# Kernel optimization log

Hardware: AMD Instinct MI355X
Metric: run time of the kernel (lower is better)

## Reference

```python
import jax, jax.numpy as jnp
import numpy as np

M, N, D, P = 16, 2048, 128, 8192
H = N // D  # 16
MAXLEN = 8448
EPS = 1e-5


def layernorm(x, g, b):
    mu = jnp.mean(x, axis=-1, keepdims=True)
    var = jnp.mean(jnp.square(x - mu), axis=-1, keepdims=True)
    return (x - mu) * jax.lax.rsqrt(var + EPS) * g + b


def setup_inputs() -> dict:
    key = jax.random.key(0)
    ks = jax.random.split(key, 10)
    s = 1.0 / np.sqrt(N)  # keep activations O(1) like trained weights
    return {
        "X": jax.random.normal(ks[0], (M, N), jnp.float32),
        "ln1_g": jnp.ones((N,), jnp.float32),
        "ln1_b": jnp.zeros((N,), jnp.float32),
        "Wq": jax.random.normal(ks[1], (N, N), jnp.float32) * s,
        "Wk": jax.random.normal(ks[2], (N, N), jnp.float32) * s,
        "Wv": jax.random.normal(ks[3], (N, N), jnp.float32) * s,
        "Wo": jax.random.normal(ks[4], (N, N), jnp.float32) * s,
        "ln2_g": jnp.ones((N,), jnp.float32),
        "ln2_b": jnp.zeros((N,), jnp.float32),
        "Wup": jax.random.normal(ks[5], (4 * N, N), jnp.float32) * s,
        "Wdown": jax.random.normal(ks[6], (N, 4 * N), jnp.float32) * (1.0 / np.sqrt(4 * N)),
        "cache_K": jax.random.normal(ks[7], (H, MAXLEN, D), jnp.float32),
        "cache_V": jax.random.normal(ks[8], (H, MAXLEN, D), jnp.float32),
    }


def reference(X, ln1_g, ln1_b, Wq, Wk, Wv, Wo, ln2_g, ln2_b, Wup, Wdown, cache_K, cache_V):
    residual = X
    Xn = layernorm(X, ln1_g, ln1_b)
    # torch Linear: y = x @ W.T
    q = (Xn @ Wq.T).reshape(M, H, D).transpose(1, 0, 2)  # (H,M,D)
    k = (Xn @ Wk.T).reshape(M, H, D).transpose(1, 0, 2)
    v = (Xn @ Wv.T).reshape(M, H, D).transpose(1, 0, 2)
    # KV-cache append
    cache_K = jax.lax.dynamic_update_slice(cache_K, k, (0, P, 0))
    cache_V = jax.lax.dynamic_update_slice(cache_V, v, (0, P, 0))
    Kc = cache_K[:, : P + M, :]  # (H,T,D), T = P+M
    Vc = cache_V[:, : P + M, :]
    scores = jnp.einsum("hmd,htd->hmt", q, Kc) / np.sqrt(D)
    weights = jax.nn.softmax(scores, axis=-1)
    attn = jnp.einsum("hmt,htd->hmd", weights, Vc)  # (H,M,D)
    attn = attn.transpose(1, 0, 2).reshape(M, N)
    X = residual + attn @ Wo.T
    residual = X
    Xn = layernorm(X, ln2_g, ln2_b)
    ffn = jax.nn.gelu(Xn @ Wup.T, approximate=False) @ Wdown.T
    return residual + ffn
```

## Files before the change

### kernel.cpp

```cpp
#include <hip/hip_runtime.h>
#include <hip/hip_bf16.h>
#include <math.h>

#define M_TOK 16
#define NDIM  2048
#define DHEAD 128
#define NHEAD 16
#define MAXLEN 8448
#define FFN   8192
#define TC    128
#define NCH   65
#define LN_EPS 1e-5f
#define RSQRT_D 0.08838834764831845f

template<int H>
__device__ __forceinline__ void fold_step(float* v, int lane, int o) {
    bool hi = (lane & o) != 0;
    #pragma unroll
    for (int i = 0; i < H; ++i) {
        float send = hi ? v[i] : v[i + H];
        float keep = hi ? v[i + H] : v[i];
        v[i] = keep + __shfl_xor(send, o);
    }
}

__device__ __forceinline__ void fold64(float* v, int lane) {
    fold_step<32>(v, lane, 32);
    fold_step<16>(v, lane, 16);
    fold_step<8>(v, lane, 8);
    fold_step<4>(v, lane, 4);
    fold_step<2>(v, lane, 2);
    fold_step<1>(v, lane, 1);
}

template<int KDIM>
__device__ __forceinline__ void gemv_splitk(const float* __restrict__ A,
                                            const float* __restrict__ W,
                                            int col0, int wid, int lane,
                                            float* v) {
    const int kbase = wid * (KDIM / 4);
    const float* wp = W + (size_t)col0 * KDIM + kbase + lane * 4;
    const float* ap = A + kbase + lane * 4;
    #pragma unroll 1
    for (int kc = 0; kc < KDIM / 4; kc += 256) {
        float4 w4[4];
        #pragma unroll
        for (int c = 0; c < 4; ++c)
            w4[c] = *(const float4*)(wp + (size_t)c * KDIM + kc);
        #pragma unroll
        for (int m = 0; m < 16; ++m) {
            float4 x4 = *(const float4*)(ap + (size_t)m * KDIM + kc);
            #pragma unroll
            for (int c = 0; c < 4; ++c) {
                v[m * 4 + c] = fmaf(w4[c].x, x4.x, v[m * 4 + c]);
                v[m * 4 + c] = fmaf(w4[c].y, x4.y, v[m * 4 + c]);
                v[m * 4 + c] = fmaf(w4[c].z, x4.z, v[m * 4 + c]);
                v[m * 4 + c] = fmaf(w4[c].w, x4.w, v[m * 4 + c]);
            }
        }
    }
}

__device__ __forceinline__ float crosswave_reduce(float val, int wid, int lane,
                                                  float (*s_red)[64]) {
    if (wid != 0) s_red[wid - 1][lane] = val;
    __syncthreads();
    return val + s_red[0][lane] + s_red[1][lane] + s_red[2][lane];
}

__global__ __launch_bounds__(256) void k_qkv(const float* __restrict__ Xn,
                                             const float* __restrict__ Wq,
                                             const float* __restrict__ Wk,
                                             const float* __restrict__ Wv,
                                             float* __restrict__ qws,
                                             float* __restrict__ kws,
                                             float* __restrict__ vws) {
    __shared__ float s_red[3][64];
    int tid = threadIdx.x, wid = tid >> 6, lane = tid & 63;
    int b = blockIdx.x;
    int sel = b >> 9;
    int cb = (b & 511) * 4;
    const float* W = (sel == 0) ? Wq : (sel == 1) ? Wk : Wv;
    float* dst = (sel == 0) ? qws : (sel == 1) ? kws : vws;
    float v[64];
    #pragma unroll
    for (int i = 0; i < 64; ++i) v[i] = 0.f;
    gemv_splitk<2048>(Xn, W, cb, wid, lane, v);
    fold64(v, lane);
    float r = crosswave_reduce(v[0], wid, lane, s_red);
    if (wid == 0) {
        int m = lane >> 2, c = lane & 3;
        int gcol = cb + c;
        int h = gcol >> 7, d = gcol & 127;
        dst[(((size_t)h * 16 + m) << 7) + d] = r;
    }
}

__device__ __forceinline__ float gelu_exact(float x) {
    return 0.5f * x * (1.0f + erff(x * 0.7071067811865475f));
}

__global__ __launch_bounds__(256) void k_up(const float* __restrict__ A,
                                            const float* __restrict__ W,
                                            float* __restrict__ out) {
    __shared__ float s_red[3][64];
    int tid = threadIdx.x, wid = tid >> 6, lane = tid & 63;
    int cb = blockIdx.x * 4;
    float v[64];
    #pragma unroll
    for (int i = 0; i < 64; ++i) v[i] = 0.f;
    gemv_splitk<2048>(A, W, cb, wid, lane, v);
    fold64(v, lane);
    float r = crosswave_reduce(v[0], wid, lane, s_red);
    if (wid == 0) {
        int m = lane >> 2, c = lane & 3;
        out[(size_t)m * FFN + cb + c] = gelu_exact(r);
    }
}

template<int KDIM>
__global__ __launch_bounds__(256) void k_resid(const float* __restrict__ A,
                                               const float* __restrict__ W,
                                               const float* __restrict__ R,
                                               float* __restrict__ out) {
    __shared__ float s_red[3][64];
    int tid = threadIdx.x, wid = tid >> 6, lane = tid & 63;
    int cb = blockIdx.x * 4;
    float v[64];
    #pragma unroll
    for (int i = 0; i < 64; ++i) v[i] = 0.f;
    gemv_splitk<KDIM>(A, W, cb, wid, lane, v);
    fold64(v, lane);
    float r = crosswave_reduce(v[0], wid, lane, s_red);
    if (wid == 0) {
        int m = lane >> 2, c = lane & 3;
        int col = cb + c;
        out[(size_t)m * NDIM + col] = R[(size_t)m * NDIM + col] + r;
    }
}

__global__ __launch_bounds__(256) void k_ln(const float* __restrict__ X,
                                            const float* __restrict__ g,
                                            const float* __restrict__ b,
                                            float* __restrict__ out) {
    int row = blockIdx.x, tid = threadIdx.x;
    const float4* xp = (const float4*)(X + (size_t)row * NDIM);
    float4 v0 = xp[tid], v1 = xp[tid + 256];
    float s = v0.x + v0.y + v0.z + v0.w + v1.x + v1.y + v1.z + v1.w;
    float q = v0.x*v0.x + v0.y*v0.y + v0.z*v0.z + v0.w*v0.w
            + v1.x*v1.x + v1.y*v1.y + v1.z*v1.z + v1.w*v1.w;
    #pragma unroll
    for (int o = 32; o; o >>= 1) { s += __shfl_xor(s, o); q += __shfl_xor(q, o); }
    __shared__ float ls[4], lq[4];
    int wid = tid >> 6, lane = tid & 63;
    if (lane == 0) { ls[wid] = s; lq[wid] = q; }
    __syncthreads();
    s = ls[0] + ls[1] + ls[2] + ls[3];
    q = lq[0] + lq[1] + lq[2] + lq[3];
    float mu  = s * (1.f / NDIM);
    float var = q * (1.f / NDIM) - mu * mu;
    float rs  = rsqrtf(var + LN_EPS);
    float4 g0 = ((const float4*)g)[tid], g1 = ((const float4*)g)[tid + 256];
    float4 b0 = ((const float4*)b)[tid], b1 = ((const float4*)b)[tid + 256];
    float4 o0, o1;
    o0.x = (v0.x - mu) * rs * g0.x + b0.x;  o0.y = (v0.y - mu) * rs * g0.y + b0.y;
    o0.z = (v0.z - mu) * rs * g0.z + b0.z;  o0.w = (v0.w - mu) * rs * g0.w + b0.w;
    o1.x = (v1.x - mu) * rs * g1.x + b1.x;  o1.y = (v1.y - mu) * rs * g1.y + b1.y;
    o1.z = (v1.z - mu) * rs * g1.z + b1.z;  o1.w = (v1.w - mu) * rs * g1.w + b1.w;
    float4* op = (float4*)(out + (size_t)row * NDIM);
    op[tid] = o0; op[tid + 256] = o1;
}

__global__ __launch_bounds__(256) void k_attn(const float* __restrict__ cacheK,
                                              const float* __restrict__ cacheV,
                                              const float* __restrict__ qws,
                                              const float* __restrict__ kws,
                                              const float* __restrict__ vws,
                                              float* __restrict__ part,
                                              float* __restrict__ ms) {
    __shared__ float s_q[16 * DHEAD];
    __shared__ float s_p[16][TC];
    int bid = blockIdx.x;
    int h = bid / NCH, c = bid % NCH;
    int nT = (c < NCH - 1) ? TC : M_TOK;
    const float* Kb = (c < NCH - 1) ? cacheK + ((size_t)h * MAXLEN + (size_t)c * TC) * DHEAD
                                    : kws + (size_t)h * M_TOK * DHEAD;
    const float* Vb = (c < NCH - 1) ? cacheV + ((size_t)h * MAXLEN + (size_t)c * TC) * DHEAD
                                    : vws + (size_t)h * M_TOK * DHEAD;
    int tid = threadIdx.x, wid = tid >> 6, lane = tid & 63;

    {
        const float4* qp = (const float4*)(qws + (size_t)h * M_TOK * DHEAD);
        float4* sq = (float4*)s_q;
        sq[tid] = qp[tid];
        sq[tid + 256] = qp[tid + 256];
    }
    __syncthreads();

    int tloc = lane & 15, ds = lane >> 4;

    if (nT == TC) {
        int t0 = wid * 32;
        const float4* kp0 = (const float4*)(Kb + (size_t)(t0 + tloc) * DHEAD + ds * 32);
        const float4* kp1 = (const float4*)(Kb + (size_t)(t0 + 16 + tloc) * DHEAD + ds * 32);
        float4 k0[8], k1[8];
        #pragma unroll
        for (int i = 0; i < 8; ++i) k0[i] = kp0[i];
        #pragma unroll
        for (int i = 0; i < 8; ++i) k1[i] = kp1[i];
        #pragma unroll 4
        for (int m = 0; m < 16; ++m) {
            const float4* qp4 = (const float4*)(s_q + m * DHEAD + ds * 32);
            float a00 = 0.f, a01 = 0.f, a02 = 0.f, a03 = 0.f;
            float a10 = 0.f, a11 = 0.f, a12 = 0.f, a13 = 0.f;
            #pragma unroll
            for (int i = 0; i < 8; ++i) {
                float4 q4 = qp4[i];
                a00 = fmaf(k0[i].x, q4.x, a00); a01 = fmaf(k0[i].y, q4.y, a01);
                a02 = fmaf(k0[i].z, q4.z, a02); a03 = fmaf(k0[i].w, q4.w, a03);
                a10 = fmaf(k1[i].x, q4.x, a10); a11 = fmaf(k1[i].y, q4.y, a11);
                a12 = fmaf(k1[i].z, q4.z, a12); a13 = fmaf(k1[i].w, q4.w, a13);
            }
            float s0 = (a00 + a01) + (a02 + a03);
            float s1 = (a10 + a11) + (a12 + a13);
            s0 += __shfl_xor(s0, 16); s0 += __shfl_xor(s0, 32);
            s1 += __shfl_xor(s1, 16); s1 += __shfl_xor(s1, 32);
            if (lane < 16) {
                s_p[m][t0 + lane]      = s0 * RSQRT_D;
                s_p[m][t0 + 16 + lane] = s1 * RSQRT_D;
            }
        }
    } else if (wid == 0) {
        const float4* kp0 = (const float4*)(Kb + (size_t)tloc * DHEAD + ds * 32);
        float4 k0[8];
        #pragma unroll
        for (int i = 0; i < 8; ++i) k0[i] = kp0[i];
        #pragma unroll 4
        for (int m = 0; m < 16; ++m) {
            const float4* qp4 = (const float4*)(s_q + m * DHEAD + ds * 32);
            float a00 = 0.f, a01 = 0.f, a02 = 0.f, a03 = 0.f;
            #pragma unroll
            for (int i = 0; i < 8; ++i) {
                float4 q4 = qp4[i];
                a00 = fmaf(k0[i].x, q4.x, a00); a01 = fmaf(k0[i].y, q4.y, a01);
                a02 = fmaf(k0[i].z, q4.z, a02); a03 = fmaf(k0[i].w, q4.w, a03);
            }
            float s0 = (a00 + a01) + (a02 + a03);
            s0 += __shfl_xor(s0, 16); s0 += __shfl_xor(s0, 32);
            if (lane < 16) s_p[m][lane] = s0 * RSQRT_D;
        }
    }
    __syncthreads();

    int m2 = tid >> 4, tl = tid & 15;
    float mx = -1e30f;
    for (int t = tl; t < nT; t += 16) mx = fmaxf(mx, s_p[m2][t]);
    #pragma unroll
    for (int o = 8; o; o >>= 1) mx = fmaxf(mx, __shfl_xor(mx, o));
    float sm = 0.f;
    for (int t = tl; t < nT; t += 16) {
        float p = expf(s_p[m2][t] - mx);
        s_p[m2][t] = p;
        sm += p;
    }
    #pragma unroll
    for (int o = 8; o; o >>= 1) sm += __shfl_xor(sm, o);
    if (tl == 0) {
        float* msp = ms + ((size_t)(h * NCH + c) * 16 + m2) * 2;
        msp[0] = mx; msp[1] = sm;
    }
    __syncthreads();

    int mg = wid * 4;
    float2 acc2[4] = {{0.f,0.f},{0.f,0.f},{0.f,0.f},{0.f,0.f}};
    for (int t = 0; t < nT; t += 8) {
        float2 vv[8];
        #pragma unroll
        for (int i = 0; i < 8; ++i)
            vv[i] = *(const float2*)(Vb + (size_t)(t + i) * DHEAD + 2 * lane);
        float4 p0[4], p1[4];
        #pragma unroll
        for (int mm = 0; mm < 4; ++mm) {
            p0[mm] = *(const float4*)&s_p[mg + mm][t];
            p1[mm] = *(const float4*)&s_p[mg + mm][t + 4];
        }
        #pragma unroll
        for (int mm = 0; mm < 4; ++mm) {
            acc2[mm].x = fmaf(p0[mm].x, vv[0].x, acc2[mm].x);
            acc2[mm].y = fmaf(p0[mm].x, vv[0].y, acc2[mm].y);
            acc2[mm].x = fmaf(p0[mm].y, vv[1].x, acc2[mm].x);
            acc2[mm].y = fmaf(p0[mm].y, vv[1].y, acc2[mm].y);
            acc2[mm].x = fmaf(p0[mm].z, vv[2].x, acc2[mm].x);
            acc2[mm].y = fmaf(p0[mm].z, vv[2].y, acc2[mm].y);
            acc2[mm].x = fmaf(p0[mm].w, vv[3].x, acc2[mm].x);
            acc2[mm].y = fmaf(p0[mm].w, vv[3].y, acc2[mm].y);
            acc2[mm].x = fmaf(p1[mm].x, vv[4].x, acc2[mm].x);
            acc2[mm].y = fmaf(p1[mm].x, vv[4].y, acc2[mm].y);
            acc2[mm].x = fmaf(p1[mm].y, vv[5].x, acc2[mm].x);
            acc2[mm].y = fmaf(p1[mm].y, vv[5].y, acc2[mm].y);
            acc2[mm].x = fmaf(p1[mm].z, vv[6].x, acc2[mm].x);
            acc2[mm].y = fmaf(p1[mm].z, vv[6].y, acc2[mm].y);
            acc2[mm].x = fmaf(p1[mm].w, vv[7].x, acc2[mm].x);
            acc2[mm].y = fmaf(p1[mm].w, vv[7].y, acc2[mm].y);
        }
    }
    #pragma unroll
    for (int mm = 0; mm < 4; ++mm) {
        float* dp = part + ((size_t)(h * NCH + c) * 16 + mg + mm) * DHEAD + 2 * lane;
        dp[0] = acc2[mm].x; dp[1] = acc2[mm].y;
    }
}

__global__ __launch_bounds__(256) void k_combine(const float* __restrict__ part,
                                                 const float* __restrict__ ms,
                                                 float* __restrict__ attnout) {
    __shared__ float scale[16][NCH];
    int h = blockIdx.x >> 3, dblk = blockIdx.x & 7;
    int tid = threadIdx.x;
    if (tid < 16) {
        int m = tid;
        float gmax = -1e30f;
        for (int c = 0; c < NCH; ++c)
            gmax = fmaxf(gmax, ms[((size_t)(h * NCH + c) * 16 + m) * 2]);
        float denom = 0.f;
        for (int c = 0; c < NCH; ++c) {
            const float* msp = ms + ((size_t)(h * NCH + c) * 16 + m) * 2;
            denom += msp[1] * expf(msp[0] - gmax);
        }
        float inv = 1.f / denom;
        for (int c = 0; c < NCH; ++c) {
            const float* msp = ms + ((size_t)(h * NCH + c) * 16 + m) * 2;
            scale[m][c] = expf(msp[0] - gmax) * inv;
        }
    }
    __syncthreads();
    int m = tid >> 4, dd = tid & 15;
    int d = dblk * 16 + dd;
    const float* pp = part + ((size_t)h * NCH * 16 + m) * DHEAD + d;
    float acc = 0.f;
    for (int c = 0; c < NCH; ++c)
        acc = fmaf(pp[(size_t)c * 16 * DHEAD], scale[m][c], acc);
    attnout[(size_t)m * NDIM + h * DHEAD + d] = acc;
}

extern "C" void kernel_launch(void* const* d_in, const int* in_sizes, int n_in,
                              void* d_out, int out_size, void* d_ws, size_t ws_size,
                              hipStream_t stream) {
    const float* X      = (const float*)d_in[0];
    const float* ln1_g  = (const float*)d_in[1];
    const float* ln1_b  = (const float*)d_in[2];
    const float* Wq     = (const float*)d_in[3];
    const float* Wk     = (const float*)d_in[4];
    const float* Wv     = (const float*)d_in[5];
    const float* Wo     = (const float*)d_in[6];
    const float* ln2_g  = (const float*)d_in[7];
    const float* ln2_b  = (const float*)d_in[8];
    const float* Wup    = (const float*)d_in[9];
    const float* Wdown  = (const float*)d_in[10];
    const float* cacheK = (const float*)d_in[11];
    const float* cacheV = (const float*)d_in[12];
    float* out = (float*)d_out;

    float* ws = (float*)d_ws;
    float* Xn1    = ws;
    float* qws    = Xn1 + 32768;
    float* kws    = qws + 32768;
    float* vws    = kws + 32768;
    float* partb  = vws + 32768;
    float* msb    = partb + 2129920;
    float* attn_o = msb + 33280;
    float* X2     = attn_o + 32768;
    float* Xn2    = X2 + 32768;
    float* ffnh   = Xn2 + 32768;

    k_ln<<<M_TOK, 256, 0, stream>>>(X, ln1_g, ln1_b, Xn1);
    k_qkv<<<1536, 256, 0, stream>>>(Xn1, Wq, Wk, Wv, qws, kws, vws);
    k_attn<<<NHEAD * NCH, 256, 0, stream>>>(cacheK, cacheV, qws, kws, vws, partb, msb);
    k_combine<<<NHEAD * 8, 256, 0, stream>>>(partb, msb, attn_o);
    k_resid<2048><<<512, 256, 0, stream>>>(attn_o, Wo, X, X2);
    k_ln<<<M_TOK, 256, 0, stream>>>(X2, ln2_g, ln2_b, Xn2);
    k_up<<<2048, 256, 0, stream>>>(Xn2, Wup, ffnh);
    k_resid<8192><<<512, 256, 0, stream>>>(ffnh, Wdown, X2, out);
}
```

Before: 165.2 us.

## Halve attention chunk size and residual GEMV columns per block to double grid size

Attention KV chunks shrink from 128 to 64 tokens, so each wave handles 16 tokens and the grid roughly doubles to 133 chunks per head. The residual GEMV kernels now compute 2 output columns per block instead of 4, using a new 32-wide fold and launching 1024 blocks. The aim is more parallelism across CUs and fewer registers per thread in the memory-bound phases. The cost is more partial results for the combine step and less weight reuse per block.

```diff
diff --git a/kernel.cpp b/kernel.cpp
--- a/kernel.cpp
+++ b/kernel.cpp
@@ -8,8 +8,8 @@
 #define NHEAD 16
 #define MAXLEN 8448
 #define FFN   8192
-#define TC    128
-#define NCH   65
+#define TC    64
+#define NCH   133
 #define LN_EPS 1e-5f
 #define RSQRT_D 0.08838834764831845f
 
@@ -31,6 +31,15 @@
     fold_step<4>(v, lane, 4);
     fold_step<2>(v, lane, 2);
     fold_step<1>(v, lane, 1);
+}
+
+__device__ __forceinline__ void fold32(float* v, int lane) {
+    fold_step<16>(v, lane, 32);
+    fold_step<8>(v, lane, 16);
+    fold_step<4>(v, lane, 8);
+    fold_step<2>(v, lane, 4);
+    fold_step<1>(v, lane, 2);
+    v[0] += __shfl_xor(v[0], 1);
 }
 
 template<int KDIM>
@@ -56,6 +65,34 @@
                 v[m * 4 + c] = fmaf(w4[c].y, x4.y, v[m * 4 + c]);
                 v[m * 4 + c] = fmaf(w4[c].z, x4.z, v[m * 4 + c]);
                 v[m * 4 + c] = fmaf(w4[c].w, x4.w, v[m * 4 + c]);
+            }
+        }
+    }
+}
+
+template<int KDIM>
+__device__ __forceinline__ void gemv_splitk2(const float* __restrict__ A,
+                                             const float* __restrict__ W,
+                                             int col0, int wid, int lane,
+                                             float* v) {
+    const int kbase = wid * (KDIM / 4);
+    const float* wp = W + (size_t)col0 * KDIM + kbase + lane * 4;
+    const float* ap = A + kbase + lane * 4;
+    #pragma unroll 1
+    for (int kc = 0; kc < KDIM / 4; kc += 256) {
+        float4 w4[2];
+        #pragma unroll
+        for (int c = 0; c < 2; ++c)
+            w4[c] = *(const float4*)(wp + (size_t)c * KDIM + kc);
+        #pragma unroll
+        for (int m = 0; m < 16; ++m) {
+            float4 x4 = *(const float4*)(ap + (size_t)m * KDIM + kc);
+            #pragma unroll
+            for (int c = 0; c < 2; ++c) {
+                v[m * 2 + c] = fmaf(w4[c].x, x4.x, v[m * 2 + c]);
+                v[m * 2 + c] = fmaf(w4[c].y, x4.y, v[m * 2 + c]);
+                v[m * 2 + c] = fmaf(w4[c].z, x4.z, v[m * 2 + c]);
+                v[m * 2 + c] = fmaf(w4[c].w, x4.w, v[m * 2 + c]);
             }
         }
     }
@@ -125,15 +162,16 @@
                                                float* __restrict__ out) {
     __shared__ float s_red[3][64];
     int tid = threadIdx.x, wid = tid >> 6, lane = tid & 63;
-    int cb = blockIdx.x * 4;
-    float v[64];
-    #pragma unroll
-    for (int i = 0; i < 64; ++i) v[i] = 0.f;
-    gemv_splitk<KDIM>(A, W, cb, wid, lane, v);
-    fold64(v, lane);
+    int cb = blockIdx.x * 2;
+    float v[32];
+    #pragma unroll
+    for (int i = 0; i < 32; ++i) v[i] = 0.f;
+    gemv_splitk2<KDIM>(A, W, cb, wid, lane, v);
+    fold32(v, lane);
     float r = crosswave_reduce(v[0], wid, lane, s_red);
-    if (wid == 0) {
-        int m = lane >> 2, c = lane & 3;
+    if (wid == 0 && (lane & 1) == 0) {
+        int idx = (lane >> 1) & 31;
+        int m = idx >> 1, c = idx & 1;
         int col = cb + c;
         out[(size_t)m * NDIM + col] = R[(size_t)m * NDIM + col] + r;
     }
@@ -199,39 +237,9 @@
 
     int tloc = lane & 15, ds = lane >> 4;
 
-    if (nT == TC) {
-        int t0 = wid * 32;
+    if (nT == TC || wid == 0) {
+        int t0 = (nT == TC) ? wid * 16 : 0;
         const float4* kp0 = (const float4*)(Kb + (size_t)(t0 + tloc) * DHEAD + ds * 32);
-        const float4* kp1 = (const float4*)(Kb + (size_t)(t0 + 16 + tloc) * DHEAD + ds * 32);
-        float4 k0[8], k1[8];
-        #pragma unroll
-        for (int i = 0; i < 8; ++i) k0[i] = kp0[i];
-        #pragma unroll
-        for (int i = 0; i < 8; ++i) k1[i] = kp1[i];
-        #pragma unroll 4
-        for (int m = 0; m < 16; ++m) {
-            const float4* qp4 = (const float4*)(s_q + m * DHEAD + ds * 32);
-            float a00 = 0.f, a01 = 0.f, a02 = 0.f, a03 = 0.f;
-            float a10 = 0.f, a11 = 0.f, a12 = 0.f, a13 = 0.f;
-            #pragma unroll
-            for (int i = 0; i < 8; ++i) {
-                float4 q4 = qp4[i];
-                a00 = fmaf(k0[i].x, q4.x, a00); a01 = fmaf(k0[i].y, q4.y, a01);
-                a02 = fmaf(k0[i].z, q4.z, a02); a03 = fmaf(k0[i].w, q4.w, a03);
-                a10 = fmaf(k1[i].x, q4.x, a10); a11 = fmaf(k1[i].y, q4.y, a11);
-                a12 = fmaf(k1[i].z, q4.z, a12); a13 = fmaf(k1[i].w, q4.w, a13);
-            }
-            float s0 = (a00 + a01) + (a02 + a03);
-            float s1 = (a10 + a11) + (a12 + a13);
-            s0 += __shfl_xor(s0, 16); s0 += __shfl_xor(s0, 32);
-            s1 += __shfl_xor(s1, 16); s1 += __shfl_xor(s1, 32);
-            if (lane < 16) {
-                s_p[m][t0 + lane]      = s0 * RSQRT_D;
-                s_p[m][t0 + 16 + lane] = s1 * RSQRT_D;
-            }
-        }
-    } else if (wid == 0) {
-        const float4* kp0 = (const float4*)(Kb + (size_t)tloc * DHEAD + ds * 32);
         float4 k0[8];
         #pragma unroll
         for (int i = 0; i < 8; ++i) k0[i] = kp0[i];
@@ -247,7 +255,7 @@
             }
             float s0 = (a00 + a01) + (a02 + a03);
             s0 += __shfl_xor(s0, 16); s0 += __shfl_xor(s0, 32);
-            if (lane < 16) s_p[m][lane] = s0 * RSQRT_D;
+            if (lane < 16) s_p[m][t0 + lane] = s0 * RSQRT_D;
         }
     }
     __syncthreads();
@@ -367,8 +375,8 @@
     float* kws    = qws + 32768;
     float* vws    = kws + 32768;
     float* partb  = vws + 32768;
-    float* msb    = partb + 2129920;
-    float* attn_o = msb + 33280;
+    float* msb    = partb + 4358144;
+    float* attn_o = msb + 68096;
     float* X2     = attn_o + 32768;
     float* Xn2    = X2 + 32768;
     float* ffnh   = Xn2 + 32768;
@@ -377,8 +385,8 @@
     k_qkv<<<1536, 256, 0, stream>>>(Xn1, Wq, Wk, Wv, qws, kws, vws);
     k_attn<<<NHEAD * NCH, 256, 0, stream>>>(cacheK, cacheV, qws, kws, vws, partb, msb);
     k_combine<<<NHEAD * 8, 256, 0, stream>>>(partb, msb, attn_o);
-    k_resid<2048><<<512, 256, 0, stream>>>(attn_o, Wo, X, X2);
+    k_resid<2048><<<1024, 256, 0, stream>>>(attn_o, Wo, X, X2);
     k_ln<<<M_TOK, 256, 0, stream>>>(X2, ln2_g, ln2_b, Xn2);
     k_up<<<2048, 256, 0, stream>>>(Xn2, Wup, ffnh);
-    k_resid<8192><<<512, 256, 0, stream>>>(ffnh, Wdown, X2, out);
-}
+    k_resid<8192><<<1024, 256, 0, stream>>>(ffnh, Wdown, X2, out);
+}
```

After: 194.3 us. 1.18x slower.

## Stream K/V tiles through LDS with async global_load_lds double buffering

Applied to the files above, without the earlier changes.

The attention kernel now loads K and V in 16-token tiles directly into padded, double-buffered LDS using global_load_lds, prefetching two tiles ahead with explicit vmcnt waits and barriers. The QK and PV loops consume one tile at a time, so HBM traffic for V overlaps the QK and softmax phases. The combine kernel also parallelises the scale computation across 16 lanes per row with shuffles and uses fast exp. The gain depends on overlapping cache reads, at the cost of more barriers and hand-written waitcnt logic that could be fragile.

```diff
diff --git a/kernel.cpp b/kernel.cpp
--- a/kernel.cpp
+++ b/kernel.cpp
@@ -12,6 +12,13 @@
 #define NCH   65
 #define LN_EPS 1e-5f
 #define RSQRT_D 0.08838834764831845f
+
+#define AS1 __attribute__((address_space(1)))
+#define AS3 __attribute__((address_space(3)))
+
+__device__ __forceinline__ void gload_lds16(const float* g, float* l) {
+    __builtin_amdgcn_global_load_lds((AS1 void*)g, (AS3 void*)l, 16, 0, 0);
+}
 
 template<int H>
 __device__ __forceinline__ void fold_step(float* v, int lane, int o) {
@@ -178,159 +185,162 @@
                                               const float* __restrict__ vws,
                                               float* __restrict__ part,
                                               float* __restrict__ ms) {
-    __shared__ float s_q[16 * DHEAD];
-    __shared__ float s_p[16][TC];
+    __shared__ float s_k[2][2080];
+    __shared__ float s_v[2][2080];
+    __shared__ float s_q[16 * 144];
+    __shared__ float s_p[16][132];
     int bid = blockIdx.x;
     int h = bid / NCH, c = bid % NCH;
     int nT = (c < NCH - 1) ? TC : M_TOK;
+    int NST = nT >> 4;
     const float* Kb = (c < NCH - 1) ? cacheK + ((size_t)h * MAXLEN + (size_t)c * TC) * DHEAD
                                     : kws + (size_t)h * M_TOK * DHEAD;
     const float* Vb = (c < NCH - 1) ? cacheV + ((size_t)h * MAXLEN + (size_t)c * TC) * DHEAD
                                     : vws + (size_t)h * M_TOK * DHEAD;
-    int tid = threadIdx.x, wid = tid >> 6, lane = tid & 63;
+    int tid = threadIdx.x, w = tid >> 6, lane = tid & 63;
+    int tloc = lane & 15, ds = lane >> 4;
 
     {
         const float4* qp = (const float4*)(qws + (size_t)h * M_TOK * DHEAD);
-        float4* sq = (float4*)s_q;
-        sq[tid] = qp[tid];
-        sq[tid + 256] = qp[tid + 256];
-    }
-    __syncthreads();
-
-    int tloc = lane & 15, ds = lane >> 4;
-
-    if (nT == TC) {
-        int t0 = wid * 32;
-        const float4* kp0 = (const float4*)(Kb + (size_t)(t0 + tloc) * DHEAD + ds * 32);
-        const float4* kp1 = (const float4*)(Kb + (size_t)(t0 + 16 + tloc) * DHEAD + ds * 32);
-        float4 k0[8], k1[8];
-        #pragma unroll
-        for (int i = 0; i < 8; ++i) k0[i] = kp0[i];
-        #pragma unroll
-        for (int i = 0; i < 8; ++i) k1[i] = kp1[i];
-        #pragma unroll 4
-        for (int m = 0; m < 16; ++m) {
-            const float4* qp4 = (const float4*)(s_q + m * DHEAD + ds * 32);
-            float a00 = 0.f, a01 = 0.f, a02 = 0.f, a03 = 0.f;
-            float a10 = 0.f, a11 = 0.f, a12 = 0.f, a13 = 0.f;
+        #pragma unroll
+        for (int i = 0; i < 2; ++i) {
+            int g = i * 256 + tid;
+            float4 v = qp[g];
+            int row = g >> 5, col4 = g & 31;
+            *(float4*)&s_q[row * 144 + (col4 >> 3) * 36 + (col4 & 7) * 4] = v;
+        }
+    }
+
+    auto issue = [&](int slot) {
+        if (slot >= 2 * NST) return;
+        const float* src; float* dst;
+        if (slot < NST) { src = Kb + (size_t)slot * 16 * DHEAD; dst = s_k[slot & 1]; }
+        else { int j = slot - NST; src = Vb + (size_t)j * 16 * DHEAD; dst = s_v[j & 1]; }
+        #pragma unroll
+        for (int k = 0; k < 2; ++k) {
+            int j = w * 2 + k;
+            gload_lds16(src + j * 256 + lane * 4, dst + j * 260);
+        }
+    };
+
+    issue(0);
+    issue(1);
+    const int lastSlot = 2 * NST - 1;
+
+    for (int s = 0; s < NST; ++s) {
+        if (s == lastSlot) asm volatile("s_waitcnt vmcnt(0) lgkmcnt(0)" ::: "memory");
+        else               asm volatile("s_waitcnt vmcnt(2) lgkmcnt(0)" ::: "memory");
+        __builtin_amdgcn_s_barrier();
+        const float* kbase = s_k[s & 1] + (tloc >> 1) * 260 + (tloc & 1) * 128 + ds * 32;
+        float4 kr[8];
+        #pragma unroll
+        for (int i = 0; i < 8; ++i) kr[i] = *(const float4*)(kbase + i * 4);
+        asm volatile("s_waitcnt lgkmcnt(0)" ::: "memory");
+        __builtin_amdgcn_s_barrier();
+        issue(s + 2);
+        #pragma unroll
+        for (int mm = 0; mm < 4; ++mm) {
+            int m = w * 4 + mm;
+            const float* qrow = s_q + m * 144 + ds * 36;
+            float a0 = 0.f, a1 = 0.f, a2 = 0.f, a3 = 0.f;
             #pragma unroll
             for (int i = 0; i < 8; ++i) {
-                float4 q4 = qp4[i];
-                a00 = fmaf(k0[i].x, q4.x, a00); a01 = fmaf(k0[i].y, q4.y, a01);
-                a02 = fmaf(k0[i].z, q4.z, a02); a03 = fmaf(k0[i].w, q4.w, a03);
-                a10 = fmaf(k1[i].x, q4.x, a10); a11 = fmaf(k1[i].y, q4.y, a11);
-                a12 = fmaf(k1[i].z, q4.z, a12); a13 = fmaf(k1[i].w, q4.w, a13);
+                float4 q4 = *(const float4*)(qrow + i * 4);
+                a0 = fmaf(kr[i].x, q4.x, a0); a1 = fmaf(kr[i].y, q4.y, a1);
+                a2 = fmaf(kr[i].z, q4.z, a2); a3 = fmaf(kr[i].w, q4.w, a3);
             }
-            float s0 = (a00 + a01) + (a02 + a03);
-            float s1 = (a10 + a11) + (a12 + a13);
-            s0 += __shfl_xor(s0, 16); s0 += __shfl_xor(s0, 32);
-            s1 += __shfl_xor(s1, 16); s1 += __shfl_xor(s1, 32);
-            if (lane < 16) {
-                s_p[m][t0 + lane]      = s0 * RSQRT_D;
-                s_p[m][t0 + 16 + lane] = s1 * RSQRT_D;
+            float s0 = (a0 + a1) + (a2 + a3);
+            s0 += __shfl_xor(s0, 16);
+            s0 += __shfl_xor(s0, 32);
+            if (ds == 0) s_p[m][s * 16 + tloc] = s0 * RSQRT_D;
+        }
+    }
+
+    asm volatile("s_waitcnt lgkmcnt(0)" ::: "memory");
+    __builtin_amdgcn_s_barrier();
+    {
+        int m2 = tid >> 4, tl = tid & 15;
+        float mx = -1e30f;
+        for (int t = tl; t < nT; t += 16) mx = fmaxf(mx, s_p[m2][t]);
+        #pragma unroll
+        for (int o = 8; o; o >>= 1) mx = fmaxf(mx, __shfl_xor(mx, o));
+        float sm = 0.f;
+        for (int t = tl; t < nT; t += 16) {
+            float p = __expf(s_p[m2][t] - mx);
+            s_p[m2][t] = p;
+            sm += p;
+        }
+        #pragma unroll
+        for (int o = 8; o; o >>= 1) sm += __shfl_xor(sm, o);
+        if (tl == 0) {
+            float* msp = ms + ((size_t)(h * NCH + c) * 16 + m2) * 2;
+            msp[0] = mx; msp[1] = sm;
+        }
+    }
+
+    float2 acc[4] = {{0.f,0.f},{0.f,0.f},{0.f,0.f},{0.f,0.f}};
+    for (int j = 0; j < NST; ++j) {
+        int s = NST + j;
+        if (s == lastSlot) asm volatile("s_waitcnt vmcnt(0) lgkmcnt(0)" ::: "memory");
+        else               asm volatile("s_waitcnt vmcnt(2) lgkmcnt(0)" ::: "memory");
+        __builtin_amdgcn_s_barrier();
+        float2 vr[16];
+        const float* vbase = s_v[j & 1];
+        #pragma unroll
+        for (int r = 0; r < 16; ++r)
+            vr[r] = *(const float2*)(vbase + (r >> 1) * 260 + (r & 1) * 128 + lane * 2);
+        asm volatile("s_waitcnt lgkmcnt(0)" ::: "memory");
+        __builtin_amdgcn_s_barrier();
+        issue(s + 2);
+        #pragma unroll
+        for (int mm = 0; mm < 4; ++mm) {
+            int m = w * 4 + mm;
+            const float* prow = &s_p[m][j * 16];
+            #pragma unroll
+            for (int g4 = 0; g4 < 4; ++g4) {
+                float4 p4 = *(const float4*)(prow + g4 * 4);
+                acc[mm].x = fmaf(p4.x, vr[g4*4+0].x, acc[mm].x);
+                acc[mm].y = fmaf(p4.x, vr[g4*4+0].y, acc[mm].y);
+                acc[mm].x = fmaf(p4.y, vr[g4*4+1].x, acc[mm].x);
+                acc[mm].y = fmaf(p4.y, vr[g4*4+1].y, acc[mm].y);
+                acc[mm].x = fmaf(p4.z, vr[g4*4+2].x, acc[mm].x);
+                acc[mm].y = fmaf(p4.z, vr[g4*4+2].y, acc[mm].y);
+                acc[mm].x = fmaf(p4.w, vr[g4*4+3].x, acc[mm].x);
+                acc[mm].y = fmaf(p4.w, vr[g4*4+3].y, acc[mm].y);
             }
         }
-    } else if (wid == 0) {
-        const float4* kp0 = (const float4*)(Kb + (size_t)tloc * DHEAD + ds * 32);
-        float4 k0[8];
-        #pragma unroll
-        for (int i = 0; i < 8; ++i) k0[i] = kp0[i];
-        #pragma unroll 4
-        for (int m = 0; m < 16; ++m) {
-            const float4* qp4 = (const float4*)(s_q + m * DHEAD + ds * 32);
-            float a00 = 0.f, a01 = 0.f, a02 = 0.f, a03 = 0.f;
-            #pragma unroll
-            for (int i = 0; i < 8; ++i) {
-                float4 q4 = qp4[i];
-                a00 = fmaf(k0[i].x, q4.x, a00); a01 = fmaf(k0[i].y, q4.y, a01);
-                a02 = fmaf(k0[i].z, q4.z, a02); a03 = fmaf(k0[i].w, q4.w, a03);
-            }
-            float s0 = (a00 + a01) + (a02 + a03);
-            s0 += __shfl_xor(s0, 16); s0 += __shfl_xor(s0, 32);
-            if (lane < 16) s_p[m][lane] = s0 * RSQRT_D;
-        }
-    }
-    __syncthreads();
-
-    int m2 = tid >> 4, tl = tid & 15;
-    float mx = -1e30f;
-    for (int t = tl; t < nT; t += 16) mx = fmaxf(mx, s_p[m2][t]);
-    #pragma unroll
-    for (int o = 8; o; o >>= 1) mx = fmaxf(mx, __shfl_xor(mx, o));
-    float sm = 0.f;
-    for (int t = tl; t < nT; t += 16) {
-        float p = expf(s_p[m2][t] - mx);
-        s_p[m2][t] = p;
-        sm += p;
-    }
-    #pragma unroll
-    for (int o = 8; o; o >>= 1) sm += __shfl_xor(sm, o);
-    if (tl == 0) {
-        float* msp = ms + ((size_t)(h * NCH + c) * 16 + m2) * 2;
-        msp[0] = mx; msp[1] = sm;
-    }
-    __syncthreads();
-
-    int mg = wid * 4;
-    float2 acc2[4] = {{0.f,0.f},{0.f,0.f},{0.f,0.f},{0.f,0.f}};
-    for (int t = 0; t < nT; t += 8) {
-        float2 vv[8];
-        #pragma unroll
-        for (int i = 0; i < 8; ++i)
-            vv[i] = *(const float2*)(Vb + (size_t)(t + i) * DHEAD + 2 * lane);
-        float4 p0[4], p1[4];
-        #pragma unroll
-        for (int mm = 0; mm < 4; ++mm) {
-            p0[mm] = *(const float4*)&s_p[mg + mm][t];
-            p1[mm] = *(const float4*)&s_p[mg + mm][t + 4];
-        }
-        #pragma unroll
-        for (int mm = 0; mm < 4; ++mm) {
-            acc2[mm].x = fmaf(p0[mm].x, vv[0].x, acc2[mm].x);
-            acc2[mm].y = fmaf(p0[mm].x, vv[0].y, acc2[mm].y);
-            acc2[mm].x = fmaf(p0[mm].y, vv[1].x, acc2[mm].x);
-            acc2[mm].y = fmaf(p0[mm].y, vv[1].y, acc2[mm].y);
-            acc2[mm].x = fmaf(p0[mm].z, vv[2].x, acc2[mm].x);
-            acc2[mm].y = fmaf(p0[mm].z, vv[2].y, acc2[mm].y);
-            acc2[mm].x = fmaf(p0[mm].w, vv[3].x, acc2[mm].x);
-            acc2[mm].y = fmaf(p0[mm].w, vv[3].y, acc2[mm].y);
-            acc2[mm].x = fmaf(p1[mm].x, vv[4].x, acc2[mm].x);
-            acc2[mm].y = fmaf(p1[mm].x, vv[4].y, acc2[mm].y);
-            acc2[mm].x = fmaf(p1[mm].y, vv[5].x, acc2[mm].x);
-            acc2[mm].y = fmaf(p1[mm].y, vv[5].y, acc2[mm].y);
-            acc2[mm].x = fmaf(p1[mm].z, vv[6].x, acc2[mm].x);
-            acc2[mm].y = fmaf(p1[mm].z, vv[6].y, acc2[mm].y);
-            acc2[mm].x = fmaf(p1[mm].w, vv[7].x, acc2[mm].x);
-            acc2[mm].y = fmaf(p1[mm].w, vv[7].y, acc2[mm].y);
-        }
-    }
-    #pragma unroll
-    for (int mm = 0; mm < 4; ++mm) {
-        float* dp = part + ((size_t)(h * NCH + c) * 16 + mg + mm) * DHEAD + 2 * lane;
-        dp[0] = acc2[mm].x; dp[1] = acc2[mm].y;
-    }
+    }
+
+    float* dp = part + (((size_t)(h * NCH + c) * 16) + w * 4) * DHEAD + 2 * lane;
+    #pragma unroll
+    for (int mm = 0; mm < 4; ++mm)
+        *(float2*)(dp + (size_t)mm * DHEAD) = acc[mm];
 }
 
 __global__ __launch_bounds__(256) void k_combine(const float* __restrict__ part,
                                                  const float* __restrict__ ms,
                                                  float* __restrict__ attnout) {
-    __shared__ float scale[16][NCH];
+    __shared__ float s_scale[16][NCH + 3];
     int h = blockIdx.x >> 3, dblk = blockIdx.x & 7;
     int tid = threadIdx.x;
-    if (tid < 16) {
-        int m = tid;
+    {
+        int cl = tid & 15, m = tid >> 4;
         float gmax = -1e30f;
-        for (int c = 0; c < NCH; ++c)
+        for (int c = cl; c < NCH; c += 16)
             gmax = fmaxf(gmax, ms[((size_t)(h * NCH + c) * 16 + m) * 2]);
+        #pragma unroll
+        for (int o = 8; o; o >>= 1) gmax = fmaxf(gmax, __shfl_xor(gmax, o));
         float denom = 0.f;
-        for (int c = 0; c < NCH; ++c) {
+        for (int c = cl; c < NCH; c += 16) {
             const float* msp = ms + ((size_t)(h * NCH + c) * 16 + m) * 2;
-            denom += msp[1] * expf(msp[0] - gmax);
-        }
+            denom += msp[1] * __expf(msp[0] - gmax);
+        }
+        #pragma unroll
+        for (int o = 8; o; o >>= 1) denom += __shfl_xor(denom, o);
         float inv = 1.f / denom;
-        for (int c = 0; c < NCH; ++c) {
+        for (int c = cl; c < NCH; c += 16) {
             const float* msp = ms + ((size_t)(h * NCH + c) * 16 + m) * 2;
-            scale[m][c] = expf(msp[0] - gmax) * inv;
+            s_scale[m][c] = __expf(msp[0] - gmax) * inv;
         }
     }
     __syncthreads();
@@ -338,8 +348,9 @@
     int d = dblk * 16 + dd;
     const float* pp = part + ((size_t)h * NCH * 16 + m) * DHEAD + d;
     float acc = 0.f;
+    #pragma unroll 4
     for (int c = 0; c < NCH; ++c)
-        acc = fmaf(pp[(size_t)c * 16 * DHEAD], scale[m][c], acc);
+        acc = fmaf(pp[(size_t)c * 16 * DHEAD], s_scale[m][c], acc);
     attnout[(size_t)m * NDIM + h * DHEAD + d] = acc;
 }
 
```

Result: faster. 155.6 us (-5.8%).
